# Kernel optimization log

Hardware: AMD Instinct MI355X
Metric: run time of the kernel (lower is better)

## Reference

```python
import jax, jax.numpy as jnp
import numpy as np

N = 50000      # nodes
E = 800000     # directed edges (before self-loops)
IN_DIM = 128
HID = 64
HEADS = 4
OUT_DIM = 64
NEG_SLOPE = 0.2


def setup_inputs() -> dict:
    key = jax.random.key(0)
    ks = jax.random.split(key, 14)
    glorot = lambda k, shape: jax.random.normal(k, shape, jnp.float32) * np.sqrt(2.0 / (shape[0] + shape[-1]))
    return {
        "x": jax.random.normal(ks[0], (N, IN_DIM), jnp.float32),
        "edge_index": jax.random.randint(ks[1], (2, E), 0, N, jnp.int64),
        "edge_attr": jax.random.normal(ks[2], (E, 16), jnp.float32),  # ignored (GATConv has edge_dim=None)
        # gat1: IN_DIM -> HEADS*HID
        "W1": glorot(ks[3], (IN_DIM, HEADS * HID)),
        "a_src1": glorot(ks[4], (HEADS, HID)),
        "a_dst1": glorot(ks[5], (HEADS, HID)),
        "b1": jnp.zeros((HEADS * HID,), jnp.float32),
        # gat2: HEADS*HID -> HEADS*HID
        "W2": glorot(ks[6], (HEADS * HID, HEADS * HID)),
        "a_src2": glorot(ks[7], (HEADS, HID)),
        "a_dst2": glorot(ks[8], (HEADS, HID)),
        "b2": jnp.zeros((HEADS * HID,), jnp.float32),
        # fc head
        "Wfc": glorot(ks[9], (HEADS * HID, OUT_DIM)),
        "bfc": jnp.zeros((OUT_DIM,), jnp.float32),
    }


def _gat_conv(x, src, dst, W, a_src, a_dst, b, num_nodes):
    """PyG GATConv, concat=True, add_self_loops handled by caller."""
    H, C = a_src.shape
    xh = (x @ W).reshape(-1, H, C)                         # [N, H, C]
    alpha_src = jnp.einsum('nhc,hc->nh', xh, a_src)        # [N, H]
    alpha_dst = jnp.einsum('nhc,hc->nh', xh, a_dst)
    e = jax.nn.leaky_relu(alpha_src[src] + alpha_dst[dst], NEG_SLOPE)  # [Etot, H]
    # segment softmax over incoming edges of each dst node
    m = jax.ops.segment_max(e, dst, num_segments=num_nodes)
    a = jnp.exp(e - jax.lax.stop_gradient(m)[dst])
    denom = jax.ops.segment_sum(a, dst, num_segments=num_nodes)
    alpha = a / (denom[dst] + 1e-16)                        # [Etot, H]
    msg = xh[src] * alpha[:, :, None]                       # gather + weight  [Etot, H, C]
    out = jax.ops.segment_sum(msg, dst, num_segments=num_nodes)  # scatter-agg [N, H, C]
    return out.reshape(num_nodes, H * C) + b


def reference(x, edge_index, edge_attr, W1, a_src1, a_dst1, b1,
              W2, a_src2, a_dst2, b2, Wfc, bfc):
    num_nodes = x.shape[0]
    loop = jnp.arange(num_nodes, dtype=edge_index.dtype)
    src = jnp.concatenate([edge_index[0], loop])  # add_self_loops=True (PyG default)
    dst = jnp.concatenate([edge_index[1], loop])
    h = jax.nn.relu(_gat_conv(x, src, dst, W1, a_src1, a_dst1, b1, num_nodes))
    h = jax.nn.relu(_gat_conv(h, src, dst, W2, a_src2, a_dst2, b2, num_nodes))
    return h @ Wfc + bfc
```

## Files before the change

### kernel.cpp

```cpp
#include <hip/hip_runtime.h>
#include <hip/hip_bf16.h>

#define N_NODES 50000
#define E_EDGES 800000
#define ETOT (E_EDGES + N_NODES)
#define IN_DIM 128
#define HID 64
#define HEADS 4
#define HC (HEADS * HID)
#define OUT_DIM 64
#define NEG_SLOPE 0.2f
#define SCAN_BLK 1024

using bf16x8 = __attribute__((ext_vector_type(8))) __bf16;
using f32x4  = __attribute__((ext_vector_type(4))) float;

__global__ __launch_bounds__(256) void cvt_bf16(const float* __restrict__ in,
                                                __hip_bfloat16* __restrict__ out,
                                                long n4) {
    long i = (long)blockIdx.x * 256 + threadIdx.x;
    if (i >= n4) return;
    float4 v = ((const float4*)in)[i];
    __hip_bfloat162 a, b;
    a.x = __float2bfloat16(v.x); a.y = __float2bfloat16(v.y);
    b.x = __float2bfloat16(v.z); b.y = __float2bfloat16(v.w);
    ((__hip_bfloat162*)out)[2 * i]     = a;
    ((__hip_bfloat162*)out)[2 * i + 1] = b;
}

__global__ __launch_bounds__(256) void wtrans(const float* __restrict__ W,
                                              __hip_bfloat16* __restrict__ Wt,
                                              int K, int N) {
    int i = blockIdx.x * 256 + threadIdx.x;
    if (i >= K * N) return;
    int k = i / N, n = i - k * N;
    Wt[(long)n * K + k] = __float2bfloat16(W[i]);
}

template <int K>
__global__ __launch_bounds__(256) void gemm_xh_mfma(const __hip_bfloat16* __restrict__ A,
                                                    const __hip_bfloat16* __restrict__ Bt,
                                                    __hip_bfloat16* __restrict__ Cb,
                                                    int M,
                                                    const float* __restrict__ a_src,
                                                    const float* __restrict__ a_dst,
                                                    float* __restrict__ as_,
                                                    float* __restrict__ ad_) {
    __shared__ unsigned short Atile[64][K + 8];
    const int t = threadIdx.x;
    const int h = t >> 6;
    const int lane = t & 63;
    const int l15 = lane & 15, l4 = lane >> 4;
    const int m0 = blockIdx.x * 64;

    constexpr int KB8 = K / 8;
#pragma unroll
    for (int i = 0; i < K / 32; i++) {
        int q = i * 256 + t;
        int row = q / KB8;
        int kc = (q - row * KB8) * 8;
        int gm = m0 + row;
        uint4 v = make_uint4(0, 0, 0, 0);
        if (gm < M) v = *(const uint4*)(A + (long)gm * K + kc);
        *(uint4*)&Atile[row][kc] = v;
    }
    __syncthreads();

    f32x4 acc[4][4];
#pragma unroll
    for (int i = 0; i < 4; i++)
#pragma unroll
        for (int j = 0; j < 4; j++) acc[i][j] = (f32x4)0.f;

    const __hip_bfloat16* Bp = Bt + ((long)(h * 64 + l15)) * K + l4 * 8;

#pragma unroll
    for (int kb = 0; kb < K / 32; kb++) {
        bf16x8 bfr[4];
#pragma unroll
        for (int cb = 0; cb < 4; cb++)
            bfr[cb] = *(const bf16x8*)(Bp + (long)cb * 16 * K + kb * 32);
        bf16x8 afr[4];
#pragma unroll
        for (int rb = 0; rb < 4; rb++)
            afr[rb] = *(const bf16x8*)&Atile[rb * 16 + l15][kb * 32 + l4 * 8];
#pragma unroll
        for (int rb = 0; rb < 4; rb++)
#pragma unroll
            for (int cb = 0; cb < 4; cb++)
                acc[rb][cb] = __builtin_amdgcn_mfma_f32_16x16x32_bf16(afr[rb], bfr[cb], acc[rb][cb], 0, 0, 0);
    }

    float asv[4], adv[4];
#pragma unroll
    for (int cb = 0; cb < 4; cb++) {
        asv[cb] = a_src[h * HID + cb * 16 + l15];
        adv[cb] = a_dst[h * HID + cb * 16 + l15];
    }
#pragma unroll
    for (int rb = 0; rb < 4; rb++) {
#pragma unroll
        for (int reg = 0; reg < 4; reg++) {
            int row = m0 + rb * 16 + l4 * 4 + reg;
            float ps = 0.f, pd = 0.f;
#pragma unroll
            for (int cb = 0; cb < 4; cb++) {
                ps += acc[rb][cb][reg] * asv[cb];
                pd += acc[rb][cb][reg] * adv[cb];
            }
#pragma unroll
            for (int off = 8; off; off >>= 1) {
                ps += __shfl_down(ps, off);
                pd += __shfl_down(pd, off);
            }
            if (l15 == 0 && row < M) {
                as_[row * HEADS + h] = ps;
                ad_[row * HEADS + h] = pd;
            }
        }
    }
#pragma unroll
    for (int rb = 0; rb < 4; rb++) {
#pragma unroll
        for (int cb = 0; cb < 4; cb++) {
#pragma unroll
            for (int reg = 0; reg < 4; reg++) {
                int row = m0 + rb * 16 + l4 * 4 + reg;
                int col = h * 64 + cb * 16 + l15;
                if (row < M) Cb[(long)row * HC + col] = __float2bfloat16(acc[rb][cb][reg]);
            }
        }
    }
}

__global__ __launch_bounds__(256) void gemm_fc_mfma(const __hip_bfloat16* __restrict__ A,
                                                    const __hip_bfloat16* __restrict__ Bt,
                                                    const float* __restrict__ bias,
                                                    float* __restrict__ C,
                                                    int M) {
    constexpr int K = 256;
    __shared__ unsigned short Atile[64][K + 8];
    const int t = threadIdx.x;
    const int w = t >> 6;
    const int lane = t & 63;
    const int l15 = lane & 15, l4 = lane >> 4;
    const int m0 = blockIdx.x * 64;

    constexpr int KB8 = K / 8;
#pragma unroll
    for (int i = 0; i < K / 32; i++) {
        int q = i * 256 + t;
        int row = q / KB8;
        int kc = (q - row * KB8) * 8;
        int gm = m0 + row;
        uint4 v = make_uint4(0, 0, 0, 0);
        if (gm < M) v = *(const uint4*)(A + (long)gm * K + kc);
        *(uint4*)&Atile[row][kc] = v;
    }
    __syncthreads();

    f32x4 acc[4];
#pragma unroll
    for (int j = 0; j < 4; j++) acc[j] = (f32x4)0.f;

    const __hip_bfloat16* Bp = Bt + (long)l15 * K + l4 * 8;
#pragma unroll
    for (int kb = 0; kb < K / 32; kb++) {
        bf16x8 afr = *(const bf16x8*)&Atile[w * 16 + l15][kb * 32 + l4 * 8];
#pragma unroll
        for (int cb = 0; cb < 4; cb++) {
            bf16x8 bfr = *(const bf16x8*)(Bp + (long)cb * 16 * K + kb * 32);
            acc[cb] = __builtin_amdgcn_mfma_f32_16x16x32_bf16(afr, bfr, acc[cb], 0, 0, 0);
        }
    }
#pragma unroll
    for (int cb = 0; cb < 4; cb++) {
#pragma unroll
        for (int reg = 0; reg < 4; reg++) {
            int row = m0 + w * 16 + l4 * 4 + reg;
            int col = cb * 16 + l15;
            if (row < M) C[(long)row * OUT_DIM + col] = acc[cb][reg] + bias[col];
        }
    }
}

__global__ __launch_bounds__(256) void hist_kernel(const int* __restrict__ ei,
                                                   int* __restrict__ deg) {
    int e = blockIdx.x * 256 + threadIdx.x;
    if (e >= ETOT) return;
    int d = (e < E_EDGES) ? ei[E_EDGES + e] : e - E_EDGES;
    atomicAdd(&deg[d], 1);
}

__global__ __launch_bounds__(SCAN_BLK) void scan_phase1(const int* __restrict__ deg,
                                                        int* __restrict__ rs,
                                                        int* __restrict__ partials,
                                                        int n) {
    __shared__ int tmp[SCAN_BLK];
    int i = blockIdx.x * SCAN_BLK + threadIdx.x;
    int v = (i < n) ? deg[i] : 0;
    tmp[threadIdx.x] = v;
    __syncthreads();
    for (int off = 1; off < SCAN_BLK; off <<= 1) {
        int t = (threadIdx.x >= (unsigned)off) ? tmp[threadIdx.x - off] : 0;
        __syncthreads();
        tmp[threadIdx.x] += t;
        __syncthreads();
    }
    if (i < n) rs[i] = tmp[threadIdx.x];
    if (threadIdx.x == SCAN_BLK - 1) partials[blockIdx.x] = tmp[SCAN_BLK - 1];
}

__global__ void scan_phase2(int* __restrict__ partials, int nb) {
    if (blockIdx.x == 0 && threadIdx.x == 0) {
        int s = 0;
        for (int i = 0; i < nb; i++) { s += partials[i]; partials[i] = s; }
    }
}

__global__ __launch_bounds__(SCAN_BLK) void scan_phase3(const int* __restrict__ deg,
                                                        int* __restrict__ rs,
                                                        const int* __restrict__ partials,
                                                        int n) {
    int i = blockIdx.x * SCAN_BLK + threadIdx.x;
    if (i < n) {
        int off = (blockIdx.x > 0) ? partials[blockIdx.x - 1] : 0;
        rs[i] = rs[i] + off - deg[i];
    } else if (i == n) {
        rs[n] = partials[gridDim.x - 1];
    }
}

__global__ __launch_bounds__(256) void fill_kernel(const int* __restrict__ ei,
                                                   int* __restrict__ cursor,
                                                   int* __restrict__ csr_src) {
    int e = blockIdx.x * 256 + threadIdx.x;
    if (e >= ETOT) return;
    int s, d;
    if (e < E_EDGES) { s = ei[e]; d = ei[E_EDGES + e]; }
    else             { s = d = e - E_EDGES; }
    int pos = atomicAdd(&cursor[d], 1);
    csr_src[pos] = s;
}

__global__ __launch_bounds__(256) void agg_kernel(const int* __restrict__ rs,
                                                  const int* __restrict__ csr_src,
                                                  const __hip_bfloat16* __restrict__ xh,
                                                  const float* __restrict__ as_,
                                                  const float* __restrict__ ad_,
                                                  const float* __restrict__ bias,
                                                  __hip_bfloat16* __restrict__ out) {
    int wid = threadIdx.x >> 6;
    int n = blockIdx.x * 4 + wid;
    if (n >= N_NODES) return;
    int lane = threadIdx.x & 63;
    int h = lane >> 4;
    int cq = lane;
    int beg = rs[n], end = rs[n + 1];
    float adv = ad_[n * HEADS + h];
    float acc0 = 0.f, acc1 = 0.f, acc2 = 0.f, acc3 = 0.f, wsum = 0.f;
    const uint2* xh4 = (const uint2*)xh;
#pragma unroll 4
    for (int p = beg; p < end; ++p) {
        int s = csr_src[p];
        float l = as_[s * HEADS + h] + adv;
        l = l > 0.f ? l : NEG_SLOPE * l;
        float wv = __expf(l);
        wsum += wv;
        uint2 v = xh4[(long)s * (HC / 4) + cq];
        float f0 = __uint_as_float(v.x << 16);
        float f1 = __uint_as_float(v.x & 0xffff0000u);
        float f2 = __uint_as_float(v.y << 16);
        float f3 = __uint_as_float(v.y & 0xffff0000u);
        acc0 += wv * f0;
        acc1 += wv * f1;
        acc2 += wv * f2;
        acc3 += wv * f3;
    }
    float inv = 1.f / (wsum + 1e-16f);
    float4 bi = *(const float4*)&bias[4 * lane];
    __hip_bfloat162 p01, p23;
    p01.x = __float2bfloat16(fmaxf(acc0 * inv + bi.x, 0.f));
    p01.y = __float2bfloat16(fmaxf(acc1 * inv + bi.y, 0.f));
    p23.x = __float2bfloat16(fmaxf(acc2 * inv + bi.z, 0.f));
    p23.y = __float2bfloat16(fmaxf(acc3 * inv + bi.w, 0.f));
    uint2 pk;
    pk.x = *(unsigned int*)&p01;
    pk.y = *(unsigned int*)&p23;
    *(uint2*)&out[(long)n * HC + 4 * lane] = pk;
}

extern "C" void kernel_launch(void* const* d_in, const int* in_sizes, int n_in,
                              void* d_out, int out_size, void* d_ws, size_t ws_size,
                              hipStream_t stream) {
    const float* x    = (const float*)d_in[0];
    const int*   ei   = (const int*)d_in[1];
    const float* W1   = (const float*)d_in[3];
    const float* a_s1 = (const float*)d_in[4];
    const float* a_d1 = (const float*)d_in[5];
    const float* b1   = (const float*)d_in[6];
    const float* W2   = (const float*)d_in[7];
    const float* a_s2 = (const float*)d_in[8];
    const float* a_d2 = (const float*)d_in[9];
    const float* b2   = (const float*)d_in[10];
    const float* Wfc  = (const float*)d_in[11];
    const float* bfc  = (const float*)d_in[12];
    float* out = (float*)d_out;

    char* ws = (char*)d_ws;
    size_t off = 0;
    __hip_bfloat16* xb  = (__hip_bfloat16*)(ws + off); off += (size_t)N_NODES * IN_DIM * 2;
    __hip_bfloat16* xh  = (__hip_bfloat16*)(ws + off); off += (size_t)N_NODES * HC * 2;
    __hip_bfloat16* y   = (__hip_bfloat16*)(ws + off); off += (size_t)N_NODES * HC * 2;
    __hip_bfloat16* W1t = (__hip_bfloat16*)(ws + off); off += (size_t)HC * IN_DIM * 2;
    __hip_bfloat16* W2t = (__hip_bfloat16*)(ws + off); off += (size_t)HC * HC * 2;
    __hip_bfloat16* Wft = (__hip_bfloat16*)(ws + off); off += (size_t)OUT_DIM * HC * 2;
    float* asb     = (float*)(ws + off); off += (size_t)N_NODES * HEADS * 4;
    float* adb     = (float*)(ws + off); off += (size_t)N_NODES * HEADS * 4;
    int*   deg     = (int*)(ws + off);   off += (size_t)N_NODES * 4;
    int*   rs      = (int*)(ws + off);   off += (size_t)(N_NODES + 1) * 4;
    int*   cursor  = (int*)(ws + off);   off += (size_t)N_NODES * 4;
    int*   partials= (int*)(ws + off);   off += 256 * 4;
    int*   csr_src = (int*)(ws + off);   off += (size_t)ETOT * 4;

    int mblocks = (N_NODES + 63) / 64;
    int edge_blocks  = (ETOT + 255) / 256;
    int scan_blocks  = (N_NODES + SCAN_BLK - 1) / SCAN_BLK;
    int scan_blocks3 = (N_NODES + 1 + SCAN_BLK - 1) / SCAN_BLK;
    int agg_blocks   = (N_NODES + 3) / 4;

    long x4 = (long)N_NODES * IN_DIM / 4;
    cvt_bf16<<<(int)((x4 + 255) / 256), 256, 0, stream>>>(x, xb, x4);
    wtrans<<<(IN_DIM * HC + 255) / 256, 256, 0, stream>>>(W1, W1t, IN_DIM, HC);
    wtrans<<<(HC * HC + 255) / 256, 256, 0, stream>>>(W2, W2t, HC, HC);
    wtrans<<<(HC * OUT_DIM + 255) / 256, 256, 0, stream>>>(Wfc, Wft, HC, OUT_DIM);

    hipMemsetAsync(deg, 0, (size_t)N_NODES * 4, stream);
    hist_kernel<<<edge_blocks, 256, 0, stream>>>(ei, deg);
    scan_phase1<<<scan_blocks, SCAN_BLK, 0, stream>>>(deg, rs, partials, N_NODES);
    scan_phase2<<<1, 64, 0, stream>>>(partials, scan_blocks);
    scan_phase3<<<scan_blocks3, SCAN_BLK, 0, stream>>>(deg, rs, partials, N_NODES);
    hipMemcpyAsync(cursor, rs, (size_t)N_NODES * 4, hipMemcpyDeviceToDevice, stream);
    fill_kernel<<<edge_blocks, 256, 0, stream>>>(ei, cursor, csr_src);

    gemm_xh_mfma<IN_DIM><<<mblocks, 256, 0, stream>>>(xb, W1t, xh, N_NODES, a_s1, a_d1, asb, adb);
    agg_kernel<<<agg_blocks, 256, 0, stream>>>(rs, csr_src, xh, asb, adb, b1, y);

    gemm_xh_mfma<HC><<<mblocks, 256, 0, stream>>>(y, W2t, xh, N_NODES, a_s2, a_d2, asb, adb);
    agg_kernel<<<agg_blocks, 256, 0, stream>>>(rs, csr_src, xh, asb, adb, b2, y);

    gemm_fc_mfma<<<mblocks, 256, 0, stream>>>(y, Wft, bfc, out, N_NODES);
}
```

Baseline: 440.4 us.

## Merge prep launches, fold scan phase2 into phase3, stage GEMM outputs via LDS

Merges the three weight-transpose launches into one kernel. Folds the single-thread partials scan into scan_phase3 as a wave-level shuffle scan, and has phase3 write cursor directly, which removes a launch and a device memcpy. The GEMM epilogues now stage results in shared memory so global stores are 16-byte coalesced, and the xh GEMM prefetches B fragments one k-step ahead. These trade extra LDS use and barriers for fewer launches and wider stores.

```diff
diff --git a/kernel.cpp b/kernel.cpp
--- a/kernel.cpp
+++ b/kernel.cpp
@@ -28,13 +28,25 @@
     ((__hip_bfloat162*)out)[2 * i + 1] = b;
 }
 
-__global__ __launch_bounds__(256) void wtrans(const float* __restrict__ W,
-                                              __hip_bfloat16* __restrict__ Wt,
-                                              int K, int N) {
+__global__ __launch_bounds__(256) void prep_weights(const float* __restrict__ W1,
+                                                    const float* __restrict__ W2,
+                                                    const float* __restrict__ Wfc,
+                                                    __hip_bfloat16* __restrict__ W1t,
+                                                    __hip_bfloat16* __restrict__ W2t,
+                                                    __hip_bfloat16* __restrict__ Wft) {
     int i = blockIdx.x * 256 + threadIdx.x;
-    if (i >= K * N) return;
-    int k = i / N, n = i - k * N;
-    Wt[(long)n * K + k] = __float2bfloat16(W[i]);
+    if (i < 32768) {
+        int k = i >> 8, n = i & 255;
+        W1t[n * IN_DIM + k] = __float2bfloat16(W1[i]);
+    } else if (i < 98304) {
+        int j = i - 32768;
+        int k = j >> 8, n = j & 255;
+        W2t[n * HC + k] = __float2bfloat16(W2[j]);
+    } else if (i < 114688) {
+        int j = i - 98304;
+        int k = j >> 6, n = j & 63;
+        Wft[n * HC + k] = __float2bfloat16(Wfc[j]);
+    }
 }
 
 template <int K>
@@ -46,7 +58,12 @@
                                                     const float* __restrict__ a_dst,
                                                     float* __restrict__ as_,
                                                     float* __restrict__ ad_) {
-    __shared__ unsigned short Atile[64][K + 8];
+    constexpr int LDSA = 64 * (K + 8) * 2;
+    constexpr int LDSC = 64 * HC * 2;
+    constexpr int SMEM = LDSA > LDSC ? LDSA : LDSC;
+    __shared__ char smem[SMEM];
+    unsigned short (*Atile)[K + 8] = (unsigned short (*)[K + 8])smem;
+
     const int t = threadIdx.x;
     const int h = t >> 6;
     const int lane = t & 63;
@@ -73,13 +90,18 @@
         for (int j = 0; j < 4; j++) acc[i][j] = (f32x4)0.f;
 
     const __hip_bfloat16* Bp = Bt + ((long)(h * 64 + l15)) * K + l4 * 8;
-
-#pragma unroll
-    for (int kb = 0; kb < K / 32; kb++) {
-        bf16x8 bfr[4];
-#pragma unroll
-        for (int cb = 0; cb < 4; cb++)
-            bfr[cb] = *(const bf16x8*)(Bp + (long)cb * 16 * K + kb * 32);
+    constexpr int NK = K / 32;
+    bf16x8 bcur[4], bnxt[4];
+#pragma unroll
+    for (int cb = 0; cb < 4; cb++) bcur[cb] = *(const bf16x8*)(Bp + (long)cb * 16 * K);
+
+#pragma unroll
+    for (int kb = 0; kb < NK; kb++) {
+        if (kb + 1 < NK) {
+#pragma unroll
+            for (int cb = 0; cb < 4; cb++)
+                bnxt[cb] = *(const bf16x8*)(Bp + (long)cb * 16 * K + (kb + 1) * 32);
+        }
         bf16x8 afr[4];
 #pragma unroll
         for (int rb = 0; rb < 4; rb++)
@@ -88,7 +110,9 @@
         for (int rb = 0; rb < 4; rb++)
 #pragma unroll
             for (int cb = 0; cb < 4; cb++)
-                acc[rb][cb] = __builtin_amdgcn_mfma_f32_16x16x32_bf16(afr[rb], bfr[cb], acc[rb][cb], 0, 0, 0);
+                acc[rb][cb] = __builtin_amdgcn_mfma_f32_16x16x32_bf16(afr[rb], bcur[cb], acc[rb][cb], 0, 0, 0);
+#pragma unroll
+        for (int cb = 0; cb < 4; cb++) bcur[cb] = bnxt[cb];
     }
 
     float asv[4], adv[4];
@@ -119,17 +143,31 @@
             }
         }
     }
+
+    __syncthreads();
+    unsigned short* Ct = (unsigned short*)smem;
 #pragma unroll
     for (int rb = 0; rb < 4; rb++) {
 #pragma unroll
         for (int cb = 0; cb < 4; cb++) {
 #pragma unroll
             for (int reg = 0; reg < 4; reg++) {
-                int row = m0 + rb * 16 + l4 * 4 + reg;
+                int rl = rb * 16 + l4 * 4 + reg;
                 int col = h * 64 + cb * 16 + l15;
-                if (row < M) Cb[(long)row * HC + col] = __float2bfloat16(acc[rb][cb][reg]);
+                __hip_bfloat16 bv = __float2bfloat16(acc[rb][cb][reg]);
+                Ct[rl * HC + col] = *(unsigned short*)&bv;
             }
         }
+    }
+    __syncthreads();
+#pragma unroll
+    for (int i = 0; i < 8; i++) {
+        int idx = i * 256 + t;
+        int row = idx >> 5;
+        int cc  = idx & 31;
+        int gm = m0 + row;
+        if (gm < M)
+            *(uint4*)&Cb[(long)gm * HC + cc * 8] = *(const uint4*)&Ct[row * HC + cc * 8];
     }
 }
 
@@ -139,7 +177,10 @@
                                                     float* __restrict__ C,
                                                     int M) {
     constexpr int K = 256;
-    __shared__ unsigned short Atile[64][K + 8];
+    constexpr int LDSA = 64 * (K + 8) * 2;
+    __shared__ char smem[LDSA];
+    unsigned short (*Atile)[K + 8] = (unsigned short (*)[K + 8])smem;
+
     const int t = threadIdx.x;
     const int w = t >> 6;
     const int lane = t & 63;
@@ -173,14 +214,28 @@
             acc[cb] = __builtin_amdgcn_mfma_f32_16x16x32_bf16(afr, bfr, acc[cb], 0, 0, 0);
         }
     }
+
+    __syncthreads();
+    float* Ct = (float*)smem;
 #pragma unroll
     for (int cb = 0; cb < 4; cb++) {
+        int col = cb * 16 + l15;
+        float bv = bias[col];
 #pragma unroll
         for (int reg = 0; reg < 4; reg++) {
-            int row = m0 + w * 16 + l4 * 4 + reg;
-            int col = cb * 16 + l15;
-            if (row < M) C[(long)row * OUT_DIM + col] = acc[cb][reg] + bias[col];
-        }
+            int rl = w * 16 + l4 * 4 + reg;
+            Ct[rl * OUT_DIM + col] = acc[cb][reg] + bv;
+        }
+    }
+    __syncthreads();
+#pragma unroll
+    for (int i = 0; i < 4; i++) {
+        int idx = i * 256 + t;
+        int row = idx >> 4;
+        int cc  = idx & 15;
+        int gm = m0 + row;
+        if (gm < M)
+            *(uint4*)&C[(long)gm * OUT_DIM + cc * 4] = *(const uint4*)&Ct[row * OUT_DIM + cc * 4];
     }
 }
 
@@ -211,23 +266,32 @@
     if (threadIdx.x == SCAN_BLK - 1) partials[blockIdx.x] = tmp[SCAN_BLK - 1];
 }
 
-__global__ void scan_phase2(int* __restrict__ partials, int nb) {
-    if (blockIdx.x == 0 && threadIdx.x == 0) {
-        int s = 0;
-        for (int i = 0; i < nb; i++) { s += partials[i]; partials[i] = s; }
-    }
-}
-
 __global__ __launch_bounds__(SCAN_BLK) void scan_phase3(const int* __restrict__ deg,
                                                         int* __restrict__ rs,
+                                                        int* __restrict__ cursor,
                                                         const int* __restrict__ partials,
-                                                        int n) {
+                                                        int nb, int n) {
+    __shared__ int sOff[2];
+    if (threadIdx.x < 64) {
+        int lane = threadIdx.x;
+        int v = (lane < nb) ? partials[lane] : 0;
+#pragma unroll
+        for (int off = 1; off < 64; off <<= 1) {
+            int tv = __shfl_up(v, off);
+            if (lane >= off) v += tv;
+        }
+        if ((int)blockIdx.x > 0 && lane == (int)blockIdx.x - 1) sOff[0] = v;
+        if (lane == nb - 1) sOff[1] = v;
+        if (blockIdx.x == 0 && lane == 0) sOff[0] = 0;
+    }
+    __syncthreads();
     int i = blockIdx.x * SCAN_BLK + threadIdx.x;
     if (i < n) {
-        int off = (blockIdx.x > 0) ? partials[blockIdx.x - 1] : 0;
-        rs[i] = rs[i] + off - deg[i];
+        int e = rs[i] + sOff[0] - deg[i];
+        rs[i] = e;
+        cursor[i] = e;
     } else if (i == n) {
-        rs[n] = partials[gridDim.x - 1];
+        rs[n] = sOff[1];
     }
 }
 
@@ -331,16 +395,12 @@
 
     long x4 = (long)N_NODES * IN_DIM / 4;
     cvt_bf16<<<(int)((x4 + 255) / 256), 256, 0, stream>>>(x, xb, x4);
-    wtrans<<<(IN_DIM * HC + 255) / 256, 256, 0, stream>>>(W1, W1t, IN_DIM, HC);
-    wtrans<<<(HC * HC + 255) / 256, 256, 0, stream>>>(W2, W2t, HC, HC);
-    wtrans<<<(HC * OUT_DIM + 255) / 256, 256, 0, stream>>>(Wfc, Wft, HC, OUT_DIM);
+    prep_weights<<<(114688 + 255) / 256, 256, 0, stream>>>(W1, W2, Wfc, W1t, W2t, Wft);
 
     hipMemsetAsync(deg, 0, (size_t)N_NODES * 4, stream);
     hist_kernel<<<edge_blocks, 256, 0, stream>>>(ei, deg);
     scan_phase1<<<scan_blocks, SCAN_BLK, 0, stream>>>(deg, rs, partials, N_NODES);
-    scan_phase2<<<1, 64, 0, stream>>>(partials, scan_blocks);
-    scan_phase3<<<scan_blocks3, SCAN_BLK, 0, stream>>>(deg, rs, partials, N_NODES);
-    hipMemcpyAsync(cursor, rs, (size_t)N_NODES * 4, hipMemcpyDeviceToDevice, stream);
+    scan_phase3<<<scan_blocks3, SCAN_BLK, 0, stream>>>(deg, rs, cursor, partials, scan_blocks, N_NODES);
     fill_kernel<<<edge_blocks, 256, 0, stream>>>(ei, cursor, csr_src);
 
     gemm_xh_mfma<IN_DIM><<<mblocks, 256, 0, stream>>>(xb, W1t, xh, N_NODES, a_s1, a_d1, asb, adb);
```

Result: faster. 421.5 us (-4.3%).
